# Optimization experiments

Hardware: AMD Instinct MI355X
Metric: run time of the kernel (lower is better)

The kernel has to match this reference:

```python
import jax, jax.numpy as jnp
import numpy as np

DIM = 1024
N_HEADS = 16
DIM_FF = 4096
EPS = 1e-12


def layer_norm(x, gamma, beta):
    u = jnp.mean(x, axis=-1, keepdims=True)
    s = jnp.mean((x - u) ** 2, axis=-1, keepdims=True)
    return gamma * ((x - u) / jnp.sqrt(s + EPS)) + beta


def setup_inputs() -> dict:
    key = jax.random.key(0)
    ks = jax.random.split(key, 12)
    B, S, D, F = 2, 2048, DIM, DIM_FF
    init = lambda k, shape: (jax.random.normal(k, shape, dtype=jnp.float32) * 0.02)
    return {
        "x": jax.random.normal(ks[0], (B, S, D), dtype=jnp.float32),
        "mask": jnp.ones((B, S), dtype=jnp.int32),
        "wq": init(ks[1], (D, D)), "bq": jnp.zeros((D,), jnp.float32),
        "wk": init(ks[2], (D, D)), "bk": jnp.zeros((D,), jnp.float32),
        "wv": init(ks[3], (D, D)), "bv": jnp.zeros((D,), jnp.float32),
        "wo": init(ks[4], (D, D)), "bo": jnp.zeros((D,), jnp.float32),
        "g1": jnp.ones((D,), jnp.float32), "b1": jnp.zeros((D,), jnp.float32),
        "w1": init(ks[5], (D, F)), "bf1": jnp.zeros((F,), jnp.float32),
        "w2": init(ks[6], (F, D)), "bf2": jnp.zeros((D,), jnp.float32),
        "g2": jnp.ones((D,), jnp.float32), "b2": jnp.zeros((D,), jnp.float32),
    }


def reference(x, mask, wq, bq, wk, bk, wv, bv, wo, bo, g1, b1, w1, bf1, w2, bf2, g2, b2):
    B, S, D = x.shape
    H = N_HEADS
    W = D // H
    # QKV projections -> (B, H, S, W)
    def heads(y):
        return y.reshape(B, S, H, W).transpose(0, 2, 1, 3)
    q = heads(x @ wq + bq)
    k = heads(x @ wk + bk)
    v = heads(x @ wv + bv)
    # scaled dot-product attention with additive mask (exact module math)
    scores = jnp.einsum('bhsw,bhtw->bhst', q, k) / np.sqrt(W).astype(np.float32)
    m = mask.astype(jnp.float32)[:, None, None, :]  # (B,1,1,S)
    scores = scores - 10000.0 * (1.0 - m)
    attn = jax.nn.softmax(scores, axis=-1)
    h = jnp.einsum('bhst,bhtw->bhsw', attn, v).transpose(0, 2, 1, 3).reshape(B, S, D)
    # residual + LN1
    h = layer_norm(x + (h @ wo + bo), g1, b1)
    # position-wise FFN with exact-erf GELU, residual + LN2
    ff = jax.nn.gelu(h @ w1 + bf1, approximate=False) @ w2 + bf2
    return layer_norm(h + ff, g2, b2)
```

## Files before the change

kernel.cpp:

```cpp
#include <hip/hip_runtime.h>
#include <cstdint>
#include <cstddef>

using u16 = unsigned short;
using u32 = unsigned int;
using u64 = unsigned long long;

typedef __bf16 bf16x8 __attribute__((ext_vector_type(8)));
typedef float f32x4 __attribute__((ext_vector_type(4)));

static constexpr int Bb = 2, S = 2048, D = 1024, H = 16, W = 64, F = 4096;
static constexpr int M = Bb * S;

__device__ __forceinline__ float bf2f(u16 u) {
  union { u32 i; float f; } c; c.i = ((u32)u) << 16; return c.f;
}
__device__ __forceinline__ u16 f2bf(float f) {
  union { float f; u32 i; } c; c.f = f;
  u32 i = c.i;
  u32 r = (i + 0x7fffu + ((i >> 16) & 1u)) >> 16;
  return (u16)r;
}
__device__ __forceinline__ u16 f2bf_cvt(float f) {
  __bf16 b = (__bf16)f;
  union { __bf16 b; u16 u; } c; c.b = b; return c.u;
}
__device__ __forceinline__ __bf16 u2b(u16 x) {
  union { u16 u; __bf16 b; } c; c.u = x; return c.b;
}
__device__ __forceinline__ void stv(float* p, size_t i, float v) { p[i] = v; }
__device__ __forceinline__ void stv(u16* p, size_t i, float v)   { p[i] = f2bf(v); }
__device__ __forceinline__ float ldv(const float* p, size_t i) { return p[i]; }
__device__ __forceinline__ float ldv(const u16* p, size_t i)   { return bf2f(p[i]); }

__device__ __forceinline__ void async_cp16(const u16* g, u16* l) {
  __builtin_amdgcn_global_load_lds(
      (const __attribute__((address_space(1))) void*)g,
      (__attribute__((address_space(3))) void*)l, 16, 0, 0);
}

__device__ __forceinline__ void swizzle8(int& bx, int& by) {
  int bid = blockIdx.y * gridDim.x + blockIdx.x;
  int gpr = gridDim.x >> 3;
  int grp = bid >> 6, rem = bid & 63;
  int gm = grp / gpr, gn = grp - gm * gpr;
  by = gm * 8 + (rem >> 3);
  bx = gn * 8 + (rem & 7);
}

__global__ __launch_bounds__(256) void conv_x_kernel(
    const float* __restrict__ src, u16* __restrict__ dst)
{
  int i = (blockIdx.x * 256 + threadIdx.x) * 4;
  float4 v = *(const float4*)(src + i);
  u16 r[4] = { f2bf(v.x), f2bf(v.y), f2bf(v.z), f2bf(v.w) };
  *(uint2*)(dst + i) = *(const uint2*)r;
}

__global__ __launch_bounds__(256) void transpose_w_kernel(
    const float* __restrict__ src, u16* __restrict__ dst, int K, int N)
{
  __shared__ __align__(16) u16 T[64][72];
  const int tid = threadIdx.x;
  const int n0 = blockIdx.x * 64, k0 = blockIdx.y * 64;
#pragma unroll
  for (int t = 0; t < 4; t++) {
    int idx = tid + t * 256;
    int r = idx >> 4, c4 = (idx & 15) * 4;
    float4 v = *(const float4*)(src + (size_t)(k0 + r) * N + n0 + c4);
    T[c4 + 0][r] = f2bf(v.x); T[c4 + 1][r] = f2bf(v.y);
    T[c4 + 2][r] = f2bf(v.z); T[c4 + 3][r] = f2bf(v.w);
  }
  __syncthreads();
#pragma unroll
  for (int t = 0; t < 2; t++) {
    int idx = tid + t * 256;
    int r = idx >> 3, c8 = (idx & 7) * 8;
    *(uint4*)(dst + (size_t)(n0 + r) * K + k0 + c8) = *(const uint4*)(&T[r][c8]);
  }
}

template<int EPI, typename TC>
__global__ __launch_bounds__(256) void gemm_bt(
    const u16* __restrict__ A, const u16* __restrict__ BT,
    const float* __restrict__ bias, TC* __restrict__ C,
    int N, int K, float scale)
{
  __shared__ __align__(16) u16 As[2][128 * 32];
  __shared__ __align__(16) u16 Bs[2][128 * 32];
  const int tid = threadIdx.x;
  const int wave = tid >> 6, lane = tid & 63;
  const int quad = lane >> 4, l16 = lane & 15;
  int bx, by; swizzle8(bx, by);
  const int m0 = by * 128, n0 = bx * 128;
  const int wm = (wave >> 1) * 64, wn = (wave & 1) * 64;
  const int srow = lane >> 2;
  const int skoff = (lane & 3) * 8;

  f32x4 acc[4][4] = {};

  for (int k0 = 0; k0 < K; k0 += 64) {
#pragma unroll
    for (int h = 0; h < 2; h++) {
#pragma unroll
      for (int t = 0; t < 2; t++) {
        int slot = wave * 2 + t;
        int row = slot * 16 + srow;
        const u16* ga = A  + (size_t)(m0 + row) * K + k0 + h * 32 + skoff;
        const u16* gb = BT + (size_t)(n0 + row) * K + k0 + h * 32 + skoff;
        async_cp16(ga, As[h] + slot * 512);
        async_cp16(gb, Bs[h] + slot * 512);
      }
    }
    __syncthreads();

#pragma unroll
    for (int h = 0; h < 2; h++) {
      bf16x8 af[4], bfv[4];
#pragma unroll
      for (int i = 0; i < 4; i++)
        af[i] = *(const bf16x8*)(As[h] + (wm + i * 16 + l16) * 32 + quad * 8);
#pragma unroll
      for (int j = 0; j < 4; j++)
        bfv[j] = *(const bf16x8*)(Bs[h] + (wn + j * 16 + l16) * 32 + quad * 8);
#pragma unroll
      for (int i = 0; i < 4; i++)
#pragma unroll
        for (int j = 0; j < 4; j++)
          acc[i][j] = __builtin_amdgcn_mfma_f32_16x16x32_bf16(af[i], bfv[j], acc[i][j], 0, 0, 0);
    }
    __syncthreads();
  }

#pragma unroll
  for (int i = 0; i < 4; i++) {
#pragma unroll
    for (int j = 0; j < 4; j++) {
#pragma unroll
      for (int r = 0; r < 4; r++) {
        int row = m0 + wm + i * 16 + quad * 4 + r;
        int col = n0 + wn + j * 16 + l16;
        float val = acc[i][j][r] + bias[col];
        if (EPI == 2) {
          int sel = col >> 10, c = col & 1023;
          if (sel == 0) val *= scale;
          int bb = row >> 11, ss = row & 2047;
          int hh = c >> 6,  ww = c & 63;
          u16* dst = (u16*)C + (size_t)sel * M * D;
          dst[(((size_t)(bb * H + hh) * S) + ss) * W + ww] = f2bf(val);
        } else {
          stv(C, (size_t)row * N + col, val);
        }
      }
    }
  }
}

__global__ __launch_bounds__(512, 2) void gemm256_gelu(
    const u16* __restrict__ A, const u16* __restrict__ BT,
    const float* __restrict__ bias, u16* __restrict__ C)
{
  constexpr int GN = F, GK = D, NT = GK / 64;
  __shared__ __align__(16) u16 AL[2][2][128 * 64];
  __shared__ __align__(16) u16 BL[2][2][128 * 64];
  const int tid = threadIdx.x;
  const int wave = tid >> 6, lane = tid & 63;
  const int quad = lane >> 4, l16 = lane & 15;
  const int wm = wave >> 2, wn = wave & 3;
  int bx, by; swizzle8(bx, by);
  const int m0 = by * 256, n0 = bx * 256;
  const int lr = lane >> 3;
  const int kc8 = ((lane & 7) ^ lr) * 8;
  const int xb = (l16 & 7) * 16;
  const int brow0 = (wn & 1) * 64;
  const char* abase = (const char*)&AL[0][wm][0];
  const char* bbase = (const char*)&BL[0][wn >> 1][0];
  constexpr int BUFB = 2 * 128 * 64 * 2;

  f32x4 acc[8][4] = {};

  auto stA = [&](int t, int buf) {
#pragma unroll
    for (int half = 0; half < 2; half++)
#pragma unroll
      for (int j = 0; j < 2; j++) {
        const u16* g = A + (size_t)(m0 + half * 128 + (j * 8 + wave) * 8 + lr) * GK
                         + t * 64 + kc8;
        async_cp16(g, &AL[buf][half][(j * 8 + wave) * 512]);
      }
  };
  auto stB = [&](int t, int buf, int half) {
#pragma unroll
    for (int j = 0; j < 2; j++) {
      const u16* g = BT + (size_t)(n0 + half * 128 + (j * 8 + wave) * 8 + lr) * GK
                        + t * 64 + kc8;
      async_cp16(g, &BL[buf][half][(j * 8 + wave) * 512]);
    }
  };

  stA(0, 0);
  stB(0, 0, 0); stB(0, 0, 1);
  stB(1, 1, 0); stB(1, 1, 1);
  asm volatile("s_waitcnt vmcnt(4)" ::: "memory");
  __builtin_amdgcn_s_barrier();

  bf16x8 af[4][2], bf0[2][2], bf1v[2][2];

#pragma unroll 2
  for (int t = 0; t < NT; t++) {
    const int buf = t & 1;
    const char* ab = abase + buf * BUFB;
    const char* bb = bbase + buf * BUFB;

#pragma unroll
    for (int i = 0; i < 4; i++)
#pragma unroll
      for (int s = 0; s < 2; s++)
        af[i][s] = *(const bf16x8*)(ab + (i * 16 + l16) * 128 + (((s * 4 + quad) * 16) ^ xb));
#pragma unroll
    for (int j = 0; j < 2; j++)
#pragma unroll
      for (int s = 0; s < 2; s++)
        bf0[j][s] = *(const bf16x8*)(bb + (brow0 + j * 16 + l16) * 128 + (((s * 4 + quad) * 16) ^ xb));
    stA((t + 1) & (NT - 1), buf ^ 1);
    __builtin_amdgcn_s_barrier();
    __builtin_amdgcn_s_setprio(1);
#pragma unroll
    for (int i = 0; i < 4; i++)
#pragma unroll
      for (int j = 0; j < 2; j++)
#pragma unroll
        for (int s = 0; s < 2; s++)
          acc[i][j] = __builtin_amdgcn_mfma_f32_16x16x32_bf16(af[i][s], bf0[j][s], acc[i][j], 0, 0, 0);
    __builtin_amdgcn_s_setprio(0);
    __builtin_amdgcn_s_barrier();

#pragma unroll
    for (int j = 0; j < 2; j++)
#pragma unroll
      for (int s = 0; s < 2; s++)
        bf1v[j][s] = *(const bf16x8*)(bb + (brow0 + 32 + j * 16 + l16) * 128 + (((s * 4 + quad) * 16) ^ xb));
    __builtin_amdgcn_s_barrier();
    __builtin_amdgcn_s_setprio(1);
#pragma unroll
    for (int i = 0; i < 4; i++)
#pragma unroll
      for (int j = 0; j < 2; j++)
#pragma unroll
        for (int s = 0; s < 2; s++)
          acc[i][2 + j] = __builtin_amdgcn_mfma_f32_16x16x32_bf16(af[i][s], bf1v[j][s], acc[i][2 + j], 0, 0, 0);
    __builtin_amdgcn_s_setprio(0);
    __builtin_amdgcn_s_barrier();

#pragma unroll
    for (int i = 0; i < 4; i++)
#pragma unroll
      for (int s = 0; s < 2; s++)
        af[i][s] = *(const bf16x8*)(ab + (64 + i * 16 + l16) * 128 + (((s * 4 + quad) * 16) ^ xb));
    stB((t + 2) & (NT - 1), buf, 0);
    __builtin_amdgcn_s_barrier();
    __builtin_amdgcn_s_setprio(1);
#pragma unroll
    for (int i = 0; i < 4; i++)
#pragma unroll
      for (int j = 0; j < 2; j++)
#pragma unroll
        for (int s = 0; s < 2; s++)
          acc[4 + i][2 + j] = __builtin_amdgcn_mfma_f32_16x16x32_bf16(af[i][s], bf1v[j][s], acc[4 + i][2 + j], 0, 0, 0);
    __builtin_amdgcn_s_setprio(0);
    __builtin_amdgcn_s_barrier();

    stB((t + 2) & (NT - 1), buf, 1);
    __builtin_amdgcn_s_barrier();
    __builtin_amdgcn_s_setprio(1);
#pragma unroll
    for (int i = 0; i < 4; i++)
#pragma unroll
      for (int j = 0; j < 2; j++)
#pragma unroll
        for (int s = 0; s < 2; s++)
          acc[4 + i][j] = __builtin_amdgcn_mfma_f32_16x16x32_bf16(af[i][s], bf0[j][s], acc[4 + i][j], 0, 0, 0);
    __builtin_amdgcn_s_setprio(0);
    asm volatile("s_waitcnt vmcnt(4)" ::: "memory");
    __builtin_amdgcn_s_barrier();
  }

  asm volatile("s_waitcnt vmcnt(0)" ::: "memory");

#pragma unroll
  for (int i = 0; i < 8; i++) {
#pragma unroll
    for (int j = 0; j < 4; j++) {
#pragma unroll
      for (int r = 0; r < 4; r++) {
        int row = m0 + wm * 128 + i * 16 + quad * 4 + r;
        int col = n0 + wn * 64 + j * 16 + l16;
        float val = acc[i][j][r] + bias[col];
        val = 0.5f * val * (1.0f + erff(val * 0.70710678118654752f));
        C[(size_t)row * GN + col] = f2bf(val);
      }
    }
  }
}

__global__ __launch_bounds__(512, 2) void gemm_ffn2_splitk(
    const u16* __restrict__ A, const u16* __restrict__ BT,
    float* __restrict__ P0, float* __restrict__ P1)
{
  constexpr int GK = F, NT = 32;
  __shared__ __align__(16) u16 AL[2][2][128 * 64];
  __shared__ __align__(16) u16 BL[2][128 * 64];
  const int tid = threadIdx.x;
  const int wave = tid >> 6, lane = tid & 63;
  const int quad = lane >> 4, l16 = lane & 15;
  const int wm = wave >> 1, wn = wave & 1;
  int bx, by; swizzle8(bx, by);
  const int m0 = by * 256, n0 = bx * 128;
  const int kbase = blockIdx.z * (F / 2);
  const int lr = lane >> 3;
  const int kc8 = ((lane & 7) ^ lr) * 8;
  const int xb = (l16 & 7) * 16;
  const int arow0 = (wm & 1) * 64;
  const int brow0 = wn * 64;
  const char* abase = (const char*)&AL[0][wm >> 1][0];
  const char* bbase = (const char*)&BL[0][0];
  constexpr int ABUF = 2 * 128 * 64 * 2;
  constexpr int BBUF = 128 * 64 * 2;

  f32x4 acc[4][4] = {};

  auto stA2 = [&](int t, int buf, int rp) {
#pragma unroll
    for (int rr = 0; rr < 2; rr++) {
      int rd = rp * 2 + rr;
      const u16* g = A + (size_t)(m0 + rd * 64 + wave * 8 + lr) * GK
                       + kbase + t * 64 + kc8;
      async_cp16(g, &AL[buf][rd >> 1][((rd & 1) * 8 + wave) * 512]);
    }
  };
  auto stB1 = [&](int t, int buf, int rd) {
    const u16* g = BT + (size_t)(n0 + rd * 64 + wave * 8 + lr) * GK
                      + kbase + t * 64 + kc8;
    async_cp16(g, &BL[buf][(rd * 8 + wave) * 512]);
  };

  stA2(0, 0, 0); stA2(0, 0, 1);
  stB1(0, 0, 0); stB1(0, 0, 1);
  stB1(1, 1, 0); stB1(1, 1, 1);
  asm volatile("s_waitcnt vmcnt(2)" ::: "memory");
  __builtin_amdgcn_s_barrier();

  bf16x8 af[2][2], bf0[2][2], bf1v[2][2];

#pragma unroll 2
  for (int t = 0; t < NT; t++) {
    const int buf = t & 1;
    const char* ab = abase + buf * ABUF;
    const char* bb = bbase + buf * BBUF;

#pragma unroll
    for (int i = 0; i < 2; i++)
#pragma unroll
      for (int s = 0; s < 2; s++)
        af[i][s] = *(const bf16x8*)(ab + (arow0 + i * 16 + l16) * 128 + (((s * 4 + quad) * 16) ^ xb));
#pragma unroll
    for (int j = 0; j < 2; j++)
#pragma unroll
      for (int s = 0; s < 2; s++)
        bf0[j][s] = *(const bf16x8*)(bb + (brow0 + j * 16 + l16) * 128 + (((s * 4 + quad) * 16) ^ xb));
    stA2((t + 1) & (NT - 1), buf ^ 1, 0);
    __builtin_amdgcn_s_barrier();
    __builtin_amdgcn_s_setprio(1);
#pragma unroll
    for (int i = 0; i < 2; i++)
#pragma unroll
      for (int j = 0; j < 2; j++)
#pragma unroll
        for (int s = 0; s < 2; s++)
          acc[i][j] = __builtin_amdgcn_mfma_f32_16x16x32_bf16(af[i][s], bf0[j][s], acc[i][j], 0, 0, 0);
    __builtin_amdgcn_s_setprio(0);
    __builtin_amdgcn_s_barrier();

#pragma unroll
    for (int j = 0; j < 2; j++)
#pragma unroll
      for (int s = 0; s < 2; s++)
        bf1v[j][s] = *(const bf16x8*)(bb + (brow0 + 32 + j * 16 + l16) * 128 + (((s * 4 + quad) * 16) ^ xb));
    stA2((t + 1) & (NT - 1), buf ^ 1, 1);
    __builtin_amdgcn_s_barrier();
    __builtin_amdgcn_s_setprio(1);
#pragma unroll
    for (int i = 0; i < 2; i++)
#pragma unroll
      for (int j = 0; j < 2; j++)
#pragma unroll
        for (int s = 0; s < 2; s++)
          acc[i][2 + j] = __builtin_amdgcn_mfma_f32_16x16x32_bf16(af[i][s], bf1v[j][s], acc[i][2 + j], 0, 0, 0);
    __builtin_amdgcn_s_setprio(0);
    __builtin_amdgcn_s_barrier();

#pragma unroll
    for (int i = 0; i < 2; i++)
#pragma unroll
      for (int s = 0; s < 2; s++)
        af[i][s] = *(const bf16x8*)(ab + (arow0 + 32 + i * 16 + l16) * 128 + (((s * 4 + quad) * 16) ^ xb));
    stB1((t + 2) & (NT - 1), buf, 0);
    __builtin_amdgcn_s_barrier();
    __builtin_amdgcn_s_setprio(1);
#pragma unroll
    for (int i = 0; i < 2; i++)
#pragma unroll
      for (int j = 0; j < 2; j++)
#pragma unroll
        for (int s = 0; s < 2; s++)
          acc[2 + i][2 + j] = __builtin_amdgcn_mfma_f32_16x16x32_bf16(af[i][s], bf1v[j][s], acc[2 + i][2 + j], 0, 0, 0);
    __builtin_amdgcn_s_setprio(0);
    __builtin_amdgcn_s_barrier();

    stB1((t + 2) & (NT - 1), buf, 1);
    __builtin_amdgcn_s_barrier();
    __builtin_amdgcn_s_setprio(1);
#pragma unroll
    for (int i = 0; i < 2; i++)
#pragma unroll
      for (int j = 0; j < 2; j++)
#pragma unroll
        for (int s = 0; s < 2; s++)
          acc[2 + i][j] = __builtin_amdgcn_mfma_f32_16x16x32_bf16(af[i][s], bf0[j][s], acc[2 + i][j], 0, 0, 0);
    __builtin_amdgcn_s_setprio(0);
    asm volatile("s_waitcnt vmcnt(2)" ::: "memory");
    __builtin_amdgcn_s_barrier();
  }

  asm volatile("s_waitcnt vmcnt(0)" ::: "memory");

  float* P = blockIdx.z ? P1 : P0;
#pragma unroll
  for (int i = 0; i < 4; i++) {
#pragma unroll
    for (int j = 0; j < 4; j++) {
#pragma unroll
      for (int r = 0; r < 4; r++) {
        int row = m0 + wm * 64 + i * 16 + quad * 4 + r;
        int col = n0 + wn * 64 + j * 16 + l16;
        P[(size_t)row * D + col] = acc[i][j][r];
      }
    }
  }
}

template<typename TC>
__global__ __launch_bounds__(256) void gemm_bt_n64(
    const u16* __restrict__ A, const u16* __restrict__ BT,
    const float* __restrict__ bias, TC* __restrict__ C,
    int N, int K)
{
  __shared__ __align__(16) u16 As[2][128 * 32];
  __shared__ __align__(16) u16 Bs[2][64 * 32];
  const int tid = threadIdx.x;
  const int wave = tid >> 6, lane = tid & 63;
  const int quad = lane >> 4, l16 = lane & 15;
  int bx, by; swizzle8(bx, by);
  const int m0 = by * 128, n0 = bx * 64;
  const int wm = (wave >> 1) * 64, wn = (wave & 1) * 32;
  const int srow = lane >> 2;
  const int skoff = (lane & 3) * 8;

  f32x4 acc[4][2] = {};

  for (int k0 = 0; k0 < K; k0 += 64) {
#pragma unroll
    for (int h = 0; h < 2; h++) {
#pragma unroll
      for (int t = 0; t < 2; t++) {
        int slot = wave * 2 + t;
        int row = slot * 16 + srow;
        async_cp16(A + (size_t)(m0 + row) * K + k0 + h * 32 + skoff, As[h] + slot * 512);
      }
      int row = wave * 16 + srow;
      async_cp16(BT + (size_t)(n0 + row) * K + k0 + h * 32 + skoff, Bs[h] + wave * 512);
    }
    __syncthreads();

#pragma unroll
    for (int h = 0; h < 2; h++) {
      bf16x8 af[4], bfv[2];
#pragma unroll
      for (int i = 0; i < 4; i++)
        af[i] = *(const bf16x8*)(As[h] + (wm + i * 16 + l16) * 32 + quad * 8);
#pragma unroll
      for (int j = 0; j < 2; j++)
        bfv[j] = *(const bf16x8*)(Bs[h] + (wn + j * 16 + l16) * 32 + quad * 8);
#pragma unroll
      for (int i = 0; i < 4; i++)
#pragma unroll
        for (int j = 0; j < 2; j++)
          acc[i][j] = __builtin_amdgcn_mfma_f32_16x16x32_bf16(af[i], bfv[j], acc[i][j], 0, 0, 0);
    }
    __syncthreads();
  }

#pragma unroll
  for (int i = 0; i < 4; i++) {
#pragma unroll
    for (int j = 0; j < 2; j++) {
#pragma unroll
      for (int r = 0; r < 4; r++) {
        int row = m0 + wm + i * 16 + quad * 4 + r;
        int col = n0 + wn + j * 16 + l16;
        stv(C, (size_t)row * N + col, acc[i][j][r] + bias[col]);
      }
    }
  }
}

__global__ __launch_bounds__(256) void transpose_v_kernel(
    const u16* __restrict__ v, u16* __restrict__ vt)
{
  __shared__ __align__(16) u16 T[64][72];
  const int bh = blockIdx.y, k0 = blockIdx.x * 64, tid = threadIdx.x;
#pragma unroll
  for (int it = 0; it < 2; it++) {
    int vv = tid + it * 256;
    int key = vv >> 3, w0 = (vv & 7) * 8;
    union { uint4 q; u16 e[8]; } u;
    u.q = *(const uint4*)(v + ((size_t)bh * S + k0 + key) * W + w0);
#pragma unroll
    for (int j = 0; j < 8; j++) T[w0 + j][key] = u.e[j];
  }
  __syncthreads();
#pragma unroll
  for (int it = 0; it < 2; it++) {
    int vv = tid + it * 256;
    int w = vv >> 3, koff = (vv & 7) * 8;
    *(uint4*)(vt + ((size_t)bh * W + w) * S + k0 + koff) = *(const uint4*)(&T[w][koff]);
  }
}

__global__ __launch_bounds__(256) void fattn_kernel(
    const u16* __restrict__ q, const u16* __restrict__ k,
    const u16* __restrict__ vt, const int* __restrict__ mask,
    u16* __restrict__ o_parts, float* __restrict__ l_parts)
{
  __shared__ __align__(16) u16 QP[2][128][32];
  __shared__ __align__(16) u16 Kl[2][64][32];
  __shared__ __align__(16) u16 Vl[2][64][32];

  const int tid = threadIdx.x, wave = tid >> 6, lane = tid & 63;
  const int quad = lane >> 4, l16 = lane & 15;
  const int bh = blockIdx.y, b = bh >> 4, h = bh & 15;
  const int q0 = blockIdx.x * 128;
  const int half = blockIdx.z;
  const int kbase = half * (S / 2);
  const int wq0 = wave * 32;
  const int sr  = tid >> 3;
  const int sg  = tid & 7;
  const int sp  = sg >> 2;
  const int sc0 = sg * 8;
  const int ssw = (((sg & 3) ^ ((sr >> 1) & 3)) << 3);
  const int xr = (l16 >> 1) & 3;
  const int rq = ((quad ^ xr) << 3);

#pragma unroll
  for (int t = 0; t < 4; t++) {
    int row = sr + t * 32;
    *(uint4*)(&QP[sp][row][ssw]) =
        *(const uint4*)(q + ((size_t)bh * S + q0 + row) * W + sc0);
  }
  __syncthreads();
  bf16x8 aq[2][2];
#pragma unroll
  for (int g = 0; g < 2; g++)
#pragma unroll
    for (int kc = 0; kc < 2; kc++)
      aq[g][kc] = *(const bf16x8*)(&QP[kc][wq0 + g * 16 + l16][rq]);

  bf16x8 ones;
  {
    u16 ov = (l16 == 0) ? (u16)0x3F80 : (u16)0;
#pragma unroll
    for (int j = 0; j < 8; j++) ones[j] = u2b(ov);
  }

  f32x4 o_acc[2][4] = {};
  f32x4 l_acc[2] = {};

  uint4 kr0, kr1, vr0, vr1;
  int mv;
  kr0 = *(const uint4*)(k  + ((size_t)bh * S + kbase + sr     ) * W + sc0);
  kr1 = *(const uint4*)(k  + ((size_t)bh * S + kbase + sr + 32) * W + sc0);
  vr0 = *(const uint4*)(vt + ((size_t)bh * W + sr     ) * S + kbase + sc0);
  vr1 = *(const uint4*)(vt + ((size_t)bh * W + sr + 32) * S + kbase + sc0);
  mv  = mask[b * S + kbase + lane];

  constexpr int NT = S / 128;
  for (int kt = 0; kt < NT; kt++) {
    __syncthreads();
    *(uint4*)(&Kl[sp][sr     ][ssw]) = kr0;
    *(uint4*)(&Kl[sp][sr + 32][ssw]) = kr1;
    *(uint4*)(&Vl[sp][sr     ][ssw]) = vr0;
    *(uint4*)(&Vl[sp][sr + 32][ssw]) = vr1;
    u64 km = __ballot(mv != 0);
    __syncthreads();

    if (kt + 1 < NT) {
      int kn = kbase + (kt + 1) * 64;
      kr0 = *(const uint4*)(k  + ((size_t)bh * S + kn + sr     ) * W + sc0);
      kr1 = *(const uint4*)(k  + ((size_t)bh * S + kn + sr + 32) * W + sc0);
      vr0 = *(const uint4*)(vt + ((size_t)bh * W + sr     ) * S + kn + sc0);
      vr1 = *(const uint4*)(vt + ((size_t)bh * W + sr + 32) * S + kn + sc0);
      mv  = mask[b * S + kn + lane];
    }

#pragma unroll
    for (int tn = 0; tn < 4; tn++) {
      bf16x8 bk0 = *(const bf16x8*)(&Kl[0][tn * 16 + l16][rq]);
      bf16x8 bk1 = *(const bf16x8*)(&Kl[1][tn * 16 + l16][rq]);
      u32 nib = (u32)(km >> (tn * 16 + quad * 4)) & 0xFu;
      int slotp = (((tn & 1) * 2 + (quad >> 1)) ^ xr) * 8 + (quad & 1) * 4;
#pragma unroll
      for (int g = 0; g < 2; g++) {
        f32x4 s4 = {};
        s4 = __builtin_amdgcn_mfma_f32_16x16x32_bf16(bk0, aq[g][0], s4, 0, 0, 0);
        s4 = __builtin_amdgcn_mfma_f32_16x16x32_bf16(bk1, aq[g][1], s4, 0, 0, 0);
        union { u64 u; u16 e[4]; } pw;
#pragma unroll
        for (int r = 0; r < 4; r++) {
          float pm = (float)((nib >> r) & 1u);
          pw.e[r] = f2bf_cvt(__expf(s4[r]) * pm);
        }
        *(u64*)(&QP[tn >> 1][wq0 + g * 16 + l16][slotp]) = pw.u;
      }
    }

#pragma unroll
    for (int kc = 0; kc < 2; kc++) {
      bf16x8 ap0 = *(const bf16x8*)(&QP[kc][wq0      + l16][rq]);
      bf16x8 ap1 = *(const bf16x8*)(&QP[kc][wq0 + 16 + l16][rq]);
#pragma unroll
      for (int tn = 0; tn < 4; tn++) {
        bf16x8 bv = *(const bf16x8*)(&Vl[kc][tn * 16 + l16][rq]);
        o_acc[0][tn] = __builtin_amdgcn_mfma_f32_16x16x32_bf16(ap0, bv, o_acc[0][tn], 0, 0, 0);
        o_acc[1][tn] = __builtin_amdgcn_mfma_f32_16x16x32_bf16(ap1, bv, o_acc[1][tn], 0, 0, 0);
      }
      l_acc[0] = __builtin_amdgcn_mfma_f32_16x16x32_bf16(ap0, ones, l_acc[0], 0, 0, 0);
      l_acc[1] = __builtin_amdgcn_mfma_f32_16x16x32_bf16(ap1, ones, l_acc[1], 0, 0, 0);
    }
  }

  u16* ob = o_parts + (size_t)half * M * D;
  float* lb = l_parts + (size_t)half * M * H;
#pragma unroll
  for (int g = 0; g < 2; g++) {
#pragma unroll
    for (int r = 0; r < 4; r++) {
      float lsum = __shfl(l_acc[g][r], lane & 0x30);
      int sg2 = q0 + wq0 + g * 16 + quad * 4 + r;
      if (l16 == 0) lb[((size_t)b * S + sg2) * H + h] = lsum;
#pragma unroll
      for (int tn = 0; tn < 4; tn++) {
        ob[((size_t)b * S + sg2) * D + h * W + tn * 16 + l16] = f2bf_cvt(o_acc[g][tn][r]);
      }
    }
  }
}

__global__ __launch_bounds__(256) void combine_attn(
    const u16* __restrict__ o_parts, const float* __restrict__ l_parts,
    u16* __restrict__ attn)
{
  size_t idx = ((size_t)blockIdx.x * 256 + threadIdx.x) * 8;
  int row = (int)(idx >> 10);
  int h = ((int)idx >> 6) & 15;
  float l = l_parts[(size_t)row * H + h] + l_parts[(size_t)M * H + (size_t)row * H + h];
  float inv = 1.0f / l;
  union { uint4 v; u16 e[8]; } a, bq, o;
  a.v  = *(const uint4*)(o_parts + idx);
  bq.v = *(const uint4*)(o_parts + (size_t)M * D + idx);
#pragma unroll
  for (int j = 0; j < 8; j++)
    o.e[j] = f2bf((bf2f(a.e[j]) + bf2f(bq.e[j])) * inv);
  *(uint4*)(attn + idx) = o.v;
}

template<typename TA, typename TR, typename TO>
__global__ __launch_bounds__(256) void ln_res_kernel(
    const TA* __restrict__ a, const TR* __restrict__ r,
    const float* __restrict__ g, const float* __restrict__ be,
    TO* __restrict__ out)
{
  const int tid = threadIdx.x, lane = tid & 63;
  const int row = blockIdx.x * 4 + (tid >> 6);
  const TA* ap = a + (size_t)row * D;
  const TR* rp = r + (size_t)row * D;
  float hv[16];
  float s = 0.f;
#pragma unroll
  for (int c = 0; c < 16; c++) {
    int d = c * 64 + lane;
    hv[c] = ldv(ap, d) + ldv(rp, d);
    s += hv[c];
  }
#pragma unroll
  for (int d = 1; d < 64; d <<= 1) s += __shfl_xor(s, d);
  float mean = s * (1.0f / D);
  float v = 0.f;
#pragma unroll
  for (int c = 0; c < 16; c++) { float t = hv[c] - mean; v += t * t; }
#pragma unroll
  for (int d = 1; d < 64; d <<= 1) v += __shfl_xor(v, d);
  float inv = rsqrtf(v * (1.0f / D) + 1e-12f);
#pragma unroll
  for (int c = 0; c < 16; c++) {
    int d = c * 64 + lane;
    stv(out, (size_t)row * D + d, g[d] * ((hv[c] - mean) * inv) + be[d]);
  }
}

__global__ __launch_bounds__(256) void ln_res3_kernel(
    const u16* __restrict__ a, const float* __restrict__ p0,
    const float* __restrict__ p1, const float* __restrict__ bias,
    const float* __restrict__ g, const float* __restrict__ be,
    float* __restrict__ out)
{
  const int tid = threadIdx.x, lane = tid & 63;
  const int row = blockIdx.x * 4 + (tid >> 6);
  const u16* ap = a + (size_t)row * D;
  const float* q0 = p0 + (size_t)row * D;
  const float* q1 = p1 + (size_t)row * D;
  float hv[16];
  float s = 0.f;
#pragma unroll
  for (int c = 0; c < 16; c++) {
    int d = c * 64 + lane;
    hv[c] = bf2f(ap[d]) + q0[d] + q1[d] + bias[d];
    s += hv[c];
  }
#pragma unroll
  for (int d = 1; d < 64; d <<= 1) s += __shfl_xor(s, d);
  float mean = s * (1.0f / D);
  float v = 0.f;
#pragma unroll
  for (int c = 0; c < 16; c++) { float t = hv[c] - mean; v += t * t; }
#pragma unroll
  for (int d = 1; d < 64; d <<= 1) v += __shfl_xor(v, d);
  float inv = rsqrtf(v * (1.0f / D) + 1e-12f);
#pragma unroll
  for (int c = 0; c < 16; c++) {
    int d = c * 64 + lane;
    out[(size_t)row * D + d] = g[d] * ((hv[c] - mean) * inv) + be[d];
  }
}

extern "C" void kernel_launch(void* const* d_in, const int* in_sizes, int n_in,
                              void* d_out, int out_size, void* d_ws, size_t ws_size,
                              hipStream_t stream)
{
  const float* x  = (const float*)d_in[0];
  const int* mask = (const int*)d_in[1];
  const float* wq = (const float*)d_in[2];  const float* bq  = (const float*)d_in[3];
  const float* wk = (const float*)d_in[4];  const float* bk  = (const float*)d_in[5];
  const float* wv = (const float*)d_in[6];  const float* bv  = (const float*)d_in[7];
  const float* wo = (const float*)d_in[8];  const float* bo  = (const float*)d_in[9];
  const float* g1 = (const float*)d_in[10]; const float* b1  = (const float*)d_in[11];
  const float* w1 = (const float*)d_in[12]; const float* bf1 = (const float*)d_in[13];
  const float* w2 = (const float*)d_in[14]; const float* bf2 = (const float*)d_in[15];
  const float* g2 = (const float*)d_in[16]; const float* b2  = (const float*)d_in[17];

  char* ws = (char*)d_ws;
  const size_t MB = 1024 * 1024;
  u16* wqkvT = (u16*)(ws + 0 * MB);
  u16* woT   = (u16*)(ws + 6 * MB);
  u16* w1T   = (u16*)(ws + 0 * MB);
  u16* w2T   = (u16*)(ws + 0 * MB);
  u16* xb    = (u16*)(ws + 8 * MB);
  u16* vt    = (u16*)(ws + 8 * MB);
  u16* q     = (u16*)(ws + 16 * MB);
  u16* proj  = (u16*)(ws + 16 * MB);
  u16* kb    = (u16*)(ws + 24 * MB);
  u16* vb    = (u16*)(ws + 32 * MB);
  u16* oparts = (u16*)(ws + 32 * MB);
  float* lparts = (float*)(ws + 0 * MB);
  u16* attn  = (u16*)(ws + 32 * MB);
  u16* ff1   = (u16*)(ws + 8 * MB);
  float* bqkv = (float*)(ws + 40 * MB);
  u16* h1    = (u16*)(ws + 40 * MB);
  float* part1 = (float*)(ws + 48 * MB);
  float* out = (float*)d_out;

  const bool bigws = ws_size >= (size_t)64 * MB;

  dim3 blk(256);

  conv_x_kernel<<<dim3(M * D / 1024), blk, 0, stream>>>(x, xb);
  transpose_w_kernel<<<dim3(16, 16), blk, 0, stream>>>(wq, wqkvT,            D, D);
  transpose_w_kernel<<<dim3(16, 16), blk, 0, stream>>>(wk, wqkvT + 1024*1024, D, D);
  transpose_w_kernel<<<dim3(16, 16), blk, 0, stream>>>(wv, wqkvT + 2048*1024, D, D);
  transpose_w_kernel<<<dim3(16, 16), blk, 0, stream>>>(wo, woT,              D, D);
  hipMemcpyAsync(bqkv,        bq, D * sizeof(float), hipMemcpyDeviceToDevice, stream);
  hipMemcpyAsync(bqkv + 1024, bk, D * sizeof(float), hipMemcpyDeviceToDevice, stream);
  hipMemcpyAsync(bqkv + 2048, bv, D * sizeof(float), hipMemcpyDeviceToDevice, stream);

  gemm_bt<2, u16><<<dim3(3072 / 128, M / 128), blk, 0, stream>>>(
      xb, wqkvT, bqkv, q, 3072, D, 0.125f);

  transpose_v_kernel<<<dim3(S / 64, Bb * H), blk, 0, stream>>>(vb, vt);
  fattn_kernel<<<dim3(S / 128, Bb * H, 2), blk, 0, stream>>>(
      q, kb, vt, mask, oparts, lparts);
  combine_attn<<<dim3(M * D / 2048), blk, 0, stream>>>(oparts, lparts, attn);

  gemm_bt_n64<u16><<<dim3(D / 64, M / 128), blk, 0, stream>>>(
      attn, woT, bo, proj, D, D);
  ln_res_kernel<float, u16, u16><<<dim3(M / 4), blk, 0, stream>>>(x, proj, g1, b1, h1);

  transpose_w_kernel<<<dim3(F / 64, D / 64), blk, 0, stream>>>(w1, w1T, D, F);
  gemm256_gelu<<<dim3(F / 256, M / 256), dim3(512), 0, stream>>>(
      h1, w1T, bf1, ff1);

  transpose_w_kernel<<<dim3(D / 64, F / 64), blk, 0, stream>>>(w2, w2T, F, D);
  if (bigws) {
    gemm_ffn2_splitk<<<dim3(D / 128, M / 256, 2), dim3(512), 0, stream>>>(
        ff1, w2T, out, part1);
    ln_res3_kernel<<<dim3(M / 4), blk, 0, stream>>>(h1, out, part1, bf2, g2, b2, out);
  } else {
    gemm_bt_n64<float><<<dim3(D / 64, M / 128), blk, 0, stream>>>(
        ff1, w2T, bf2, out, D, F);
    ln_res_kernel<u16, float, float><<<dim3(M / 4), blk, 0, stream>>>(h1, out, g2, b2, out);
  }
}
```

Before: 401.2 us.

## Use 256x256 pipelined GEMM for QKV and widen attention query tiles

Replaces the simple 128x128 QKV GEMM with a templated version of the tuned 256x256 8-wave GEMM already used for FFN1, with a head-scatter epilogue added. The flash-attention kernel now processes 256 query rows per block (64 per wave), so each K/V tile is reused across more queries. It also skips the mask multiply when a key chunk is fully unmasked. The QKV grid shrinks to 12x16 blocks and the attention grid halves, which may lower occupancy and raise register pressure.

Result: faster. 390.9 us (-2.6%).

```diff
diff --git a/kernel.cpp b/kernel.cpp
--- a/kernel.cpp
+++ b/kernel.cpp
@@ -80,94 +80,20 @@
   }
 }
 
-template<int EPI, typename TC>
-__global__ __launch_bounds__(256) void gemm_bt(
+template<int GN, int GK, int EPI, bool SWZ>
+__global__ __launch_bounds__(512, 2) void gemm256(
     const u16* __restrict__ A, const u16* __restrict__ BT,
-    const float* __restrict__ bias, TC* __restrict__ C,
-    int N, int K, float scale)
-{
-  __shared__ __align__(16) u16 As[2][128 * 32];
-  __shared__ __align__(16) u16 Bs[2][128 * 32];
-  const int tid = threadIdx.x;
-  const int wave = tid >> 6, lane = tid & 63;
-  const int quad = lane >> 4, l16 = lane & 15;
-  int bx, by; swizzle8(bx, by);
-  const int m0 = by * 128, n0 = bx * 128;
-  const int wm = (wave >> 1) * 64, wn = (wave & 1) * 64;
-  const int srow = lane >> 2;
-  const int skoff = (lane & 3) * 8;
-
-  f32x4 acc[4][4] = {};
-
-  for (int k0 = 0; k0 < K; k0 += 64) {
-#pragma unroll
-    for (int h = 0; h < 2; h++) {
-#pragma unroll
-      for (int t = 0; t < 2; t++) {
-        int slot = wave * 2 + t;
-        int row = slot * 16 + srow;
-        const u16* ga = A  + (size_t)(m0 + row) * K + k0 + h * 32 + skoff;
-        const u16* gb = BT + (size_t)(n0 + row) * K + k0 + h * 32 + skoff;
-        async_cp16(ga, As[h] + slot * 512);
-        async_cp16(gb, Bs[h] + slot * 512);
-      }
-    }
-    __syncthreads();
-
-#pragma unroll
-    for (int h = 0; h < 2; h++) {
-      bf16x8 af[4], bfv[4];
-#pragma unroll
-      for (int i = 0; i < 4; i++)
-        af[i] = *(const bf16x8*)(As[h] + (wm + i * 16 + l16) * 32 + quad * 8);
-#pragma unroll
-      for (int j = 0; j < 4; j++)
-        bfv[j] = *(const bf16x8*)(Bs[h] + (wn + j * 16 + l16) * 32 + quad * 8);
-#pragma unroll
-      for (int i = 0; i < 4; i++)
-#pragma unroll
-        for (int j = 0; j < 4; j++)
-          acc[i][j] = __builtin_amdgcn_mfma_f32_16x16x32_bf16(af[i], bfv[j], acc[i][j], 0, 0, 0);
-    }
-    __syncthreads();
-  }
-
-#pragma unroll
-  for (int i = 0; i < 4; i++) {
-#pragma unroll
-    for (int j = 0; j < 4; j++) {
-#pragma unroll
-      for (int r = 0; r < 4; r++) {
-        int row = m0 + wm + i * 16 + quad * 4 + r;
-        int col = n0 + wn + j * 16 + l16;
-        float val = acc[i][j][r] + bias[col];
-        if (EPI == 2) {
-          int sel = col >> 10, c = col & 1023;
-          if (sel == 0) val *= scale;
-          int bb = row >> 11, ss = row & 2047;
-          int hh = c >> 6,  ww = c & 63;
-          u16* dst = (u16*)C + (size_t)sel * M * D;
-          dst[(((size_t)(bb * H + hh) * S) + ss) * W + ww] = f2bf(val);
-        } else {
-          stv(C, (size_t)row * N + col, val);
-        }
-      }
-    }
-  }
-}
-
-__global__ __launch_bounds__(512, 2) void gemm256_gelu(
-    const u16* __restrict__ A, const u16* __restrict__ BT,
-    const float* __restrict__ bias, u16* __restrict__ C)
-{
-  constexpr int GN = F, GK = D, NT = GK / 64;
+    const float* __restrict__ bias, u16* __restrict__ C, float scale)
+{
+  constexpr int NT = GK / 64;
   __shared__ __align__(16) u16 AL[2][2][128 * 64];
   __shared__ __align__(16) u16 BL[2][2][128 * 64];
   const int tid = threadIdx.x;
   const int wave = tid >> 6, lane = tid & 63;
   const int quad = lane >> 4, l16 = lane & 15;
   const int wm = wave >> 2, wn = wave & 3;
-  int bx, by; swizzle8(bx, by);
+  int bx, by;
+  if (SWZ) { swizzle8(bx, by); } else { bx = blockIdx.x; by = blockIdx.y; }
   const int m0 = by * 256, n0 = bx * 256;
   const int lr = lane >> 3;
   const int kc8 = ((lane & 7) ^ lr) * 8;
@@ -296,8 +222,17 @@
         int row = m0 + wm * 128 + i * 16 + quad * 4 + r;
         int col = n0 + wn * 64 + j * 16 + l16;
         float val = acc[i][j][r] + bias[col];
-        val = 0.5f * val * (1.0f + erff(val * 0.70710678118654752f));
-        C[(size_t)row * GN + col] = f2bf(val);
+        if (EPI == 1) {
+          val = 0.5f * val * (1.0f + erff(val * 0.70710678118654752f));
+          C[(size_t)row * GN + col] = f2bf(val);
+        } else {
+          int sel = col >> 10, c = col & 1023;
+          if (sel == 0) val *= scale;
+          int bb2 = row >> 11, ss = row & 2047;
+          int hh = c >> 6,  ww = c & 63;
+          u16* dst = C + (size_t)sel * M * D;
+          dst[(((size_t)(bb2 * H + hh) * S) + ss) * W + ww] = f2bf(val);
+        }
       }
     }
   }
@@ -542,17 +477,17 @@
     const u16* __restrict__ vt, const int* __restrict__ mask,
     u16* __restrict__ o_parts, float* __restrict__ l_parts)
 {
-  __shared__ __align__(16) u16 QP[2][128][32];
+  __shared__ __align__(16) u16 QP[2][256][32];
   __shared__ __align__(16) u16 Kl[2][64][32];
   __shared__ __align__(16) u16 Vl[2][64][32];
 
   const int tid = threadIdx.x, wave = tid >> 6, lane = tid & 63;
   const int quad = lane >> 4, l16 = lane & 15;
   const int bh = blockIdx.y, b = bh >> 4, h = bh & 15;
-  const int q0 = blockIdx.x * 128;
+  const int q0 = blockIdx.x * 256;
   const int half = blockIdx.z;
   const int kbase = half * (S / 2);
-  const int wq0 = wave * 32;
+  const int wq0 = wave * 64;
   const int sr  = tid >> 3;
   const int sg  = tid & 7;
   const int sp  = sg >> 2;
@@ -562,15 +497,15 @@
   const int rq = ((quad ^ xr) << 3);
 
 #pragma unroll
-  for (int t = 0; t < 4; t++) {
+  for (int t = 0; t < 8; t++) {
     int row = sr + t * 32;
     *(uint4*)(&QP[sp][row][ssw]) =
         *(const uint4*)(q + ((size_t)bh * S + q0 + row) * W + sc0);
   }
   __syncthreads();
-  bf16x8 aq[2][2];
-#pragma unroll
-  for (int g = 0; g < 2; g++)
+  bf16x8 aq[4][2];
+#pragma unroll
+  for (int g = 0; g < 4; g++)
 #pragma unroll
     for (int kc = 0; kc < 2; kc++)
       aq[g][kc] = *(const bf16x8*)(&QP[kc][wq0 + g * 16 + l16][rq]);
@@ -582,8 +517,8 @@
     for (int j = 0; j < 8; j++) ones[j] = u2b(ov);
   }
 
-  f32x4 o_acc[2][4] = {};
-  f32x4 l_acc[2] = {};
+  f32x4 o_acc[4][4] = {};
+  f32x4 l_acc[4] = {};
 
   uint4 kr0, kr1, vr0, vr1;
   int mv;
@@ -612,6 +547,7 @@
       mv  = mask[b * S + kn + lane];
     }
 
+    const bool allm = (km == ~0ull);
 #pragma unroll
     for (int tn = 0; tn < 4; tn++) {
       bf16x8 bk0 = *(const bf16x8*)(&Kl[0][tn * 16 + l16][rq]);
@@ -619,15 +555,20 @@
       u32 nib = (u32)(km >> (tn * 16 + quad * 4)) & 0xFu;
       int slotp = (((tn & 1) * 2 + (quad >> 1)) ^ xr) * 8 + (quad & 1) * 4;
 #pragma unroll
-      for (int g = 0; g < 2; g++) {
+      for (int g = 0; g < 4; g++) {
         f32x4 s4 = {};
         s4 = __builtin_amdgcn_mfma_f32_16x16x32_bf16(bk0, aq[g][0], s4, 0, 0, 0);
         s4 = __builtin_amdgcn_mfma_f32_16x16x32_bf16(bk1, aq[g][1], s4, 0, 0, 0);
         union { u64 u; u16 e[4]; } pw;
-#pragma unroll
-        for (int r = 0; r < 4; r++) {
-          float pm = (float)((nib >> r) & 1u);
-          pw.e[r] = f2bf_cvt(__expf(s4[r]) * pm);
+        if (allm) {
+#pragma unroll
+          for (int r = 0; r < 4; r++) pw.e[r] = f2bf_cvt(__expf(s4[r]));
+        } else {
+#pragma unroll
+          for (int r = 0; r < 4; r++) {
+            float pm = (float)((nib >> r) & 1u);
+            pw.e[r] = f2bf_cvt(__expf(s4[r]) * pm);
+          }
         }
         *(u64*)(&QP[tn >> 1][wq0 + g * 16 + l16][slotp]) = pw.u;
       }
@@ -635,23 +576,27 @@
 
 #pragma unroll
     for (int kc = 0; kc < 2; kc++) {
-      bf16x8 ap0 = *(const bf16x8*)(&QP[kc][wq0      + l16][rq]);
-      bf16x8 ap1 = *(const bf16x8*)(&QP[kc][wq0 + 16 + l16][rq]);
+      bf16x8 ap[4];
+#pragma unroll
+      for (int g = 0; g < 4; g++)
+        ap[g] = *(const bf16x8*)(&QP[kc][wq0 + g * 16 + l16][rq]);
 #pragma unroll
       for (int tn = 0; tn < 4; tn++) {
         bf16x8 bv = *(const bf16x8*)(&Vl[kc][tn * 16 + l16][rq]);
-        o_acc[0][tn] = __builtin_amdgcn_mfma_f32_16x16x32_bf16(ap0, bv, o_acc[0][tn], 0, 0, 0);
-        o_acc[1][tn] = __builtin_amdgcn_mfma_f32_16x16x32_bf16(ap1, bv, o_acc[1][tn], 0, 0, 0);
+#pragma unroll
+        for (int g = 0; g < 4; g++)
+          o_acc[g][tn] = __builtin_amdgcn_mfma_f32_16x16x32_bf16(ap[g], bv, o_acc[g][tn], 0, 0, 0);
       }
-      l_acc[0] = __builtin_amdgcn_mfma_f32_16x16x32_bf16(ap0, ones, l_acc[0], 0, 0, 0);
-      l_acc[1] = __builtin_amdgcn_mfma_f32_16x16x32_bf16(ap1, ones, l_acc[1], 0, 0, 0);
+#pragma unroll
+      for (int g = 0; g < 4; g++)
+        l_acc[g] = __builtin_amdgcn_mfma_f32_16x16x32_bf16(ap[g], ones, l_acc[g], 0, 0, 0);
     }
   }
 
   u16* ob = o_parts + (size_t)half * M * D;
   float* lb = l_parts + (size_t)half * M * H;
 #pragma unroll
-  for (int g = 0; g < 2; g++) {
+  for (int g = 0; g < 4; g++) {
 #pragma unroll
     for (int r = 0; r < 4; r++) {
       float lsum = __shfl(l_acc[g][r], lane & 0x30);
@@ -801,11 +746,11 @@
   hipMemcpyAsync(bqkv + 1024, bk, D * sizeof(float), hipMemcpyDeviceToDevice, stream);
   hipMemcpyAsync(bqkv + 2048, bv, D * sizeof(float), hipMemcpyDeviceToDevice, stream);
 
-  gemm_bt<2, u16><<<dim3(3072 / 128, M / 128), blk, 0, stream>>>(
-      xb, wqkvT, bqkv, q, 3072, D, 0.125f);
+  gemm256<3072, 1024, 2, false><<<dim3(3072 / 256, M / 256), dim3(512), 0, stream>>>(
+      xb, wqkvT, bqkv, q, 0.125f);
 
   transpose_v_kernel<<<dim3(S / 64, Bb * H), blk, 0, stream>>>(vb, vt);
-  fattn_kernel<<<dim3(S / 128, Bb * H, 2), blk, 0, stream>>>(
+  fattn_kernel<<<dim3(S / 256, Bb * H, 2), blk, 0, stream>>>(
       q, kb, vt, mask, oparts, lparts);
   combine_attn<<<dim3(M * D / 2048), blk, 0, stream>>>(oparts, lparts, attn);
 
@@ -814,8 +759,8 @@
   ln_res_kernel<float, u16, u16><<<dim3(M / 4), blk, 0, stream>>>(x, proj, g1, b1, h1);
 
   transpose_w_kernel<<<dim3(F / 64, D / 64), blk, 0, stream>>>(w1, w1T, D, F);
-  gemm256_gelu<<<dim3(F / 256, M / 256), dim3(512), 0, stream>>>(
-      h1, w1T, bf1, ff1);
+  gemm256<4096, 1024, 1, true><<<dim3(F / 256, M / 256), dim3(512), 0, stream>>>(
+      h1, w1T, bf1, ff1, 1.0f);
 
   transpose_w_kernel<<<dim3(D / 64, F / 64), blk, 0, stream>>>(w2, w2T, F, D);
   if (bigws) {
```
